# Kernel tuning notes

Hardware: AMD Instinct MI355X
Metric: run time of the kernel (lower is better)

Reference implementation:

```python
import jax, jax.numpy as jnp
import numpy as np

N, E, IN, HID, HEADS, OUT = 50000, 800000, 128, 32, 4, 2
NEG = 0.2   # LeakyReLU negative slope (PyG default)
EPS = 1e-5  # BatchNorm eps


def setup_inputs() -> dict:
    key = jax.random.key(0)
    ks = jax.random.split(key, 32)
    g = lambda i, shape, s=0.05: (jax.random.normal(ks[i], shape, jnp.float32) * s)
    d = {
        'x': jax.random.normal(ks[0], (N, IN), jnp.float32),
        'edge_index': jax.random.randint(ks[1], (2, E), 0, N, jnp.int32),
        'edge_attr': jax.random.normal(ks[2], (E, 1), jnp.float32),
        # conv1: GATv2, in=IN, out=HID, heads=HEADS, edge_dim=1
        'c1_Wl': g(3, (IN, HEADS * HID)), 'c1_bl': g(4, (HEADS * HID,)),
        'c1_Wr': g(5, (IN, HEADS * HID)), 'c1_br': g(6, (HEADS * HID,)),
        'c1_We': g(7, (1, HEADS * HID)),
        'c1_att': g(8, (HEADS, HID)),
        'c1_bias': g(9, (HEADS * HID,)),
        'bn1_gamma': jnp.ones((HEADS * HID,), jnp.float32),
        'bn1_beta': jnp.zeros((HEADS * HID,), jnp.float32),
        'bn1_mean': g(10, (HEADS * HID,)),
        'bn1_var': jax.random.uniform(ks[11], (HEADS * HID,), jnp.float32, 0.5, 1.5),
        # conv2: GATv2, in=HEADS*HID, out=HID, heads=1, edge_dim=1
        'c2_Wl': g(12, (HEADS * HID, HID)), 'c2_bl': g(13, (HID,)),
        'c2_Wr': g(14, (HEADS * HID, HID)), 'c2_br': g(15, (HID,)),
        'c2_We': g(16, (1, HID)),
        'c2_att': g(17, (1, HID)),
        'c2_bias': g(18, (HID,)),
        'bn2_gamma': jnp.ones((HID,), jnp.float32),
        'bn2_beta': jnp.zeros((HID,), jnp.float32),
        'bn2_mean': g(19, (HID,)),
        'bn2_var': jax.random.uniform(ks[20], (HID,), jnp.float32, 0.5, 1.5),
        # classifier
        'clf_W': g(21, (HID, OUT)), 'clf_b': g(22, (OUT,)),
    }
    return d


def _gatv2(x, src, dst, eattr, Wl, bl, Wr, br, We, att, bias, heads, out_ch, concat):
    n = x.shape[0]
    xl = (x @ Wl + bl).reshape(n, heads, out_ch)   # source transform
    xr = (x @ Wr + br).reshape(n, heads, out_ch)   # target transform
    el = (eattr @ We).reshape(-1, heads, out_ch)   # edge transform (no bias in PyG)
    s = xl[src] + xr[dst] + el                     # [E, H, C]
    s = jnp.where(s > 0, s, NEG * s)               # LeakyReLU
    logits = jnp.einsum('ehc,hc->eh', s, att)      # [E, H]
    # segment softmax over destination nodes (every node has a self-loop)
    m = jax.ops.segment_max(logits, dst, num_segments=n)
    a = jnp.exp(logits - m[dst])
    denom = jax.ops.segment_sum(a, dst, num_segments=n)
    alpha = a / denom[dst]                         # [E, H]
    out = jax.ops.segment_sum(alpha[:, :, None] * xl[src], dst, num_segments=n)
    out = out.reshape(n, heads * out_ch) if concat else out.mean(axis=1)
    return out + bias


def _bn_eval(x, gamma, beta, mean, var):
    return (x - mean) * (gamma / jnp.sqrt(var + EPS)) + beta


def reference(x, edge_index, edge_attr,
              c1_Wl, c1_bl, c1_Wr, c1_br, c1_We, c1_att, c1_bias,
              bn1_gamma, bn1_beta, bn1_mean, bn1_var,
              c2_Wl, c2_bl, c2_Wr, c2_br, c2_We, c2_att, c2_bias,
              bn2_gamma, bn2_beta, bn2_mean, bn2_var,
              clf_W, clf_b):
    n = x.shape[0]
    # add self-loops once (PyG GATv2 default add_self_loops=True, fill_value='mean')
    loop = jnp.arange(n, dtype=edge_index.dtype)
    src = jnp.concatenate([edge_index[0], loop])
    dst = jnp.concatenate([edge_index[1], loop])
    loop_attr = jnp.broadcast_to(edge_attr.mean(axis=0, keepdims=True), (n, edge_attr.shape[1]))
    eattr = jnp.concatenate([edge_attr, loop_attr], axis=0)

    h = _gatv2(x, src, dst, eattr, c1_Wl, c1_bl, c1_Wr, c1_br, c1_We, c1_att, c1_bias,
               HEADS, HID, True)
    h = jax.nn.relu(_bn_eval(h, bn1_gamma, bn1_beta, bn1_mean, bn1_var))
    # dropout inactive in eval mode
    h = _gatv2(h, src, dst, eattr, c2_Wl, c2_bl, c2_Wr, c2_br, c2_We, c2_att, c2_bias,
               1, HID, True)
    h = jax.nn.relu(_bn_eval(h, bn2_gamma, bn2_beta, bn2_mean, bn2_var))
    return h @ clf_W + clf_b
```

## Files before the change

kernel.cpp:

```cpp
#include <hip/hip_runtime.h>

#define NNODES 50000
#define NEDGES 800000
#define ETOT   850000
#define IN_CH  128
#define HID    32
#define HEADS  4
#define C1     128
#define NEG    0.2f
#define BNEPS  1e-5f
#define XFB2   1563
#define EHB    3125
#define WTS    160
#define XSS    136
#define NC     16
#define SCB    196

typedef __attribute__((ext_vector_type(8))) short short8;
typedef __attribute__((ext_vector_type(4))) float f32x4;

__device__ __forceinline__ unsigned short bf16r(float f) {
    unsigned u = __float_as_uint(f);
    return (unsigned short)((u + 0x7fffu + ((u >> 16) & 1u)) >> 16);
}
__device__ __forceinline__ unsigned bf16pair(float f0, float f1) {
    return (unsigned)bf16r(f0) | ((unsigned)bf16r(f1) << 16);
}
__device__ __forceinline__ float blo(unsigned u) { return __uint_as_float(u << 16); }
__device__ __forceinline__ float bhi(unsigned u) { return __uint_as_float(u & 0xffff0000u); }

__device__ __forceinline__ int block_iscan(int v, int* ls) {
    int lane = threadIdx.x & 63, w = threadIdx.x >> 6;
    #pragma unroll
    for (int o = 1; o < 64; o <<= 1) {
        int t = __shfl_up(v, o);
        if (lane >= o) v += t;
    }
    if (lane == 63) ls[w] = v;
    __syncthreads();
    int add = 0;
    #pragma unroll
    for (int i = 0; i < 4; i++) add += (i < w) ? ls[i] : 0;
    return v + add;
}

__global__ __launch_bounds__(256) void k_prep(const float* __restrict__ Wl1,
                                              const float* __restrict__ Wr1,
                                              const float* __restrict__ Wl2,
                                              const float* __restrict__ Wr2,
                                              unsigned short* __restrict__ WT,
                                              unsigned short* __restrict__ WT2) {
    int idx = blockIdx.x * 256 + threadIdx.x;
    if (idx < 32768) {
        int mat = idx >> 14, rem = idx & 16383;
        int k = rem >> 7, n = rem & 127;
        float v = mat ? Wr1[k * 128 + n] : Wl1[k * 128 + n];
        WT[(size_t)(mat * 128 + n) * WTS + k] = bf16r(v);
    } else {
        int i2 = idx - 32768;
        int mat = i2 >> 12, rem = i2 & 4095;
        int k = rem >> 5, n = rem & 31;
        float v = mat ? Wr2[k * 32 + n] : Wl2[k * 32 + n];
        WT2[(size_t)(mat * 32 + n) * WTS + k] = bf16r(v);
    }
}

__global__ __launch_bounds__(256) void k_xf_eh(
    const float* __restrict__ x,
    const float* __restrict__ bl, const float* __restrict__ br,
    const unsigned short* __restrict__ WT,
    unsigned* __restrict__ xlb, float* __restrict__ xr,
    const int* __restrict__ ei, const float* __restrict__ ea,
    int* __restrict__ hist, float* __restrict__ meanbuf) {
    __shared__ short xs_s[64 * XSS];
    if (blockIdx.x >= XFB2) {
        float* ls = (float*)xs_s;
        int eb = blockIdx.x - XFB2;
        int e = eb * 256 + threadIdx.x;
        int c = eb & (NC - 1);
        float v = 0.f;
        if (e < NEDGES) {
            atomicAdd(&hist[c * NNODES + ei[NEDGES + e]], 1);
            v = ea[e];
        }
        #pragma unroll
        for (int o = 32; o > 0; o >>= 1) v += __shfl_down(v, o, 64);
        if ((threadIdx.x & 63) == 0) ls[threadIdx.x >> 6] = v;
        __syncthreads();
        if (threadIdx.x == 0) atomicAdd(meanbuf, ls[0] + ls[1] + ls[2] + ls[3]);
        return;
    }
    int n0g = blockIdx.x * 32;
    {
        int nd = threadIdx.x >> 3, kc = (threadIdx.x & 7) * 16;
        bool valid = (n0g + nd) < NNODES;
        float xv[16];
        #pragma unroll
        for (int i = 0; i < 4; i++) {
            float4 t = valid ? ((const float4*)(x + (size_t)(n0g + nd) * IN_CH + kc))[i]
                             : make_float4(0.f, 0.f, 0.f, 0.f);
            xv[4 * i] = t.x; xv[4 * i + 1] = t.y; xv[4 * i + 2] = t.z; xv[4 * i + 3] = t.w;
        }
        unsigned hi[8], lo[8];
        #pragma unroll
        for (int i = 0; i < 8; i++) {
            unsigned short h0 = bf16r(xv[2 * i]), h1 = bf16r(xv[2 * i + 1]);
            float l0 = xv[2 * i]     - __uint_as_float(((unsigned)h0) << 16);
            float l1 = xv[2 * i + 1] - __uint_as_float(((unsigned)h1) << 16);
            hi[i] = (unsigned)h0 | ((unsigned)h1 << 16);
            lo[i] = bf16pair(l0, l1);
        }
        uint4* ph = (uint4*)&xs_s[nd * XSS + kc];
        ph[0] = make_uint4(hi[0], hi[1], hi[2], hi[3]);
        ph[1] = make_uint4(hi[4], hi[5], hi[6], hi[7]);
        uint4* pl = (uint4*)&xs_s[(nd + 32) * XSS + kc];
        pl[0] = make_uint4(lo[0], lo[1], lo[2], lo[3]);
        pl[1] = make_uint4(lo[4], lo[5], lo[6], lo[7]);
    }
    __syncthreads();
    int lane = threadIdx.x & 63;
    int lm = lane & 15, q = lane >> 4;
    int w = threadIdx.x >> 6;
    int n0 = w * 64;
    f32x4 acc[2][4];
    #pragma unroll
    for (int mt = 0; mt < 2; mt++)
        #pragma unroll
        for (int nt = 0; nt < 4; nt++) acc[mt][nt] = (f32x4)0.f;

    #pragma unroll
    for (int ks = 0; ks < 4; ks++) {
        int k0 = ks * 32 + q * 8;
        short8 ah0 = *(const short8*)&xs_s[(lm)      * XSS + k0];
        short8 ah1 = *(const short8*)&xs_s[(16 + lm) * XSS + k0];
        short8 al0 = *(const short8*)&xs_s[(32 + lm) * XSS + k0];
        short8 al1 = *(const short8*)&xs_s[(48 + lm) * XSS + k0];
        #pragma unroll
        for (int nt = 0; nt < 4; nt++) {
            short8 bfr = *(const short8*)(WT + (size_t)(n0 + nt * 16 + lm) * WTS + k0);
            acc[0][nt] = __builtin_amdgcn_mfma_f32_16x16x32_bf16(al0, bfr, acc[0][nt], 0, 0, 0);
            acc[0][nt] = __builtin_amdgcn_mfma_f32_16x16x32_bf16(ah0, bfr, acc[0][nt], 0, 0, 0);
            acc[1][nt] = __builtin_amdgcn_mfma_f32_16x16x32_bf16(al1, bfr, acc[1][nt], 0, 0, 0);
            acc[1][nt] = __builtin_amdgcn_mfma_f32_16x16x32_bf16(ah1, bfr, acc[1][nt], 0, 0, 0);
        }
    }
    if (w < 2) {
        #pragma unroll
        for (int nt = 0; nt < 4; nt++) {
            int ch = n0 + nt * 16 + lm;
            float bv = bl[ch];
            #pragma unroll
            for (int mt = 0; mt < 2; mt++)
                #pragma unroll
                for (int r = 0; r < 4; r++) {
                    int node = n0g + mt * 16 + q * 4 + r;
                    float val = acc[mt][nt][r] + bv;
                    float pv = __shfl_xor(val, 1);
                    if ((lm & 1) == 0 && node < NNODES)
                        xlb[(size_t)node * 64 + (ch >> 1)] = bf16pair(val, pv);
                }
        }
    } else {
        #pragma unroll
        for (int nt = 0; nt < 4; nt++) {
            int ch = n0 - 128 + nt * 16 + lm;
            float bv = br[ch];
            #pragma unroll
            for (int mt = 0; mt < 2; mt++)
                #pragma unroll
                for (int r = 0; r < 4; r++) {
                    int node = n0g + mt * 16 + q * 4 + r;
                    if (node < NNODES)
                        xr[(size_t)node * C1 + ch] = acc[mt][nt][r] + bv;
                }
        }
    }
}

__global__ __launch_bounds__(256) void k_red(int* __restrict__ hist,
                                             int* __restrict__ deg,
                                             int* __restrict__ bsum) {
    __shared__ int ls[4];
    int d = blockIdx.x * 256 + threadIdx.x;
    int s = 0;
    if (d < NNODES) {
        #pragma unroll
        for (int c = 0; c < NC; c++) {
            int v = hist[c * NNODES + d];
            hist[c * NNODES + d] = s;
            s += v;
        }
        deg[d] = s;
    }
    int v = (d < NNODES) ? s + 1 : 0;
    #pragma unroll
    for (int o = 32; o > 0; o >>= 1) v += __shfl_down(v, o, 64);
    if ((threadIdx.x & 63) == 0) ls[threadIdx.x >> 6] = v;
    __syncthreads();
    if (threadIdx.x == 0) bsum[blockIdx.x] = ls[0] + ls[1] + ls[2] + ls[3];
}

__global__ __launch_bounds__(256) void k_bscan(const int* __restrict__ bsum,
                                               int* __restrict__ boff) {
    __shared__ int ls[4];
    int t = threadIdx.x;
    int v = (t < SCB) ? bsum[t] : 0;
    int incl = block_iscan(v, ls);
    if (t < SCB) boff[t] = incl - v;
}

__global__ __launch_bounds__(256) void k_rowp(const int* __restrict__ deg,
                                              const int* __restrict__ boff,
                                              int* __restrict__ rowptr) {
    __shared__ int ls[4];
    int d = blockIdx.x * 256 + threadIdx.x;
    int v = (d < NNODES) ? deg[d] + 1 : 0;
    int incl = block_iscan(v, ls);
    int base = boff[blockIdx.x];
    if (d < NNODES) rowptr[d] = base + incl - v;
    if (d == NNODES - 1) rowptr[NNODES] = base + incl;
}

__global__ __launch_bounds__(256) void k_fill(const int* __restrict__ ei,
                                              const float* __restrict__ ea,
                                              const int* __restrict__ rowptr,
                                              const float* __restrict__ meanbuf,
                                              int* __restrict__ hist,
                                              unsigned* __restrict__ cpack) {
    int e = blockIdx.x * 256 + threadIdx.x;
    if (e < NEDGES) {
        int d = ei[NEDGES + e];
        int c = (e >> 8) & (NC - 1);
        int off = atomicAdd(&hist[c * NNODES + d], 1);
        cpack[rowptr[d] + 1 + off] = ((unsigned)bf16r(ea[e]) << 16) | (unsigned)ei[e];
    } else if (e < NEDGES + NNODES) {
        int i = e - NEDGES;
        cpack[rowptr[i]] = ((unsigned)bf16r(meanbuf[0] * (1.0f / NEDGES)) << 16) | (unsigned)i;
    } else if (e < NEDGES + NNODES + 64) {
        cpack[ETOT + e - NEDGES - NNODES] = 0u;
    }
}

__global__ __launch_bounds__(256) void k_edge1(
    const unsigned* __restrict__ xlb, const float* __restrict__ xr,
    const int* __restrict__ rowptr, const unsigned* __restrict__ cpack,
    const float* __restrict__ We, const float* __restrict__ att,
    float* __restrict__ out1) {
    int node = blockIdx.x * 4 + (threadIdx.x >> 6);
    if (node >= NNODES) return;
    int lane = threadIdx.x & 63;
    int q = lane & 15, s = lane >> 4;
    int r0 = rowptr[node], r1 = rowptr[node + 1];
    float4 xr0 = ((const float4*)xr)[(size_t)node * 32 + 2 * q];
    float4 xr1 = ((const float4*)xr)[(size_t)node * 32 + 2 * q + 1];
    float4 we0 = ((const float4*)We)[2 * q],  we1 = ((const float4*)We)[2 * q + 1];
    float4 at0 = ((const float4*)att)[2 * q], at1 = ((const float4*)att)[2 * q + 1];
    const uint4* xlv = (const uint4*)xlb;

    float den = 0.f;
    float a0 = 0.f, a1 = 0.f, a2 = 0.f, a3 = 0.f;
    float a4 = 0.f, a5 = 0.f, a6 = 0.f, a7 = 0.f;
    int nit = (r1 - r0 + 3) >> 2;
    int k = r0 + s;
    unsigned sc = cpack[k];
    uint4 xv = xlv[(size_t)(sc & 0xffffu) * 16 + q];
    for (int it = 0; it < nit; it++) {
        unsigned scn = cpack[k + 4];
        uint4 xvn = xlv[(size_t)(scn & 0xffffu) * 16 + q];
        bool ok = k < r1;
        float av = __uint_as_float(sc & 0xffff0000u);
        float x0 = blo(xv.x), x1 = bhi(xv.x), x2 = blo(xv.y), x3 = bhi(xv.y);
        float x4 = blo(xv.z), x5 = bhi(xv.z), x6 = blo(xv.w), x7 = bhi(xv.w);
        float v0 = x0 + xr0.x + av * we0.x;  v0 = v0 > 0.f ? v0 : NEG * v0;
        float v1 = x1 + xr0.y + av * we0.y;  v1 = v1 > 0.f ? v1 : NEG * v1;
        float v2 = x2 + xr0.z + av * we0.z;  v2 = v2 > 0.f ? v2 : NEG * v2;
        float v3 = x3 + xr0.w + av * we0.w;  v3 = v3 > 0.f ? v3 : NEG * v3;
        float v4 = x4 + xr1.x + av * we1.x;  v4 = v4 > 0.f ? v4 : NEG * v4;
        float v5 = x5 + xr1.y + av * we1.y;  v5 = v5 > 0.f ? v5 : NEG * v5;
        float v6 = x6 + xr1.z + av * we1.z;  v6 = v6 > 0.f ? v6 : NEG * v6;
        float v7 = x7 + xr1.w + av * we1.w;  v7 = v7 > 0.f ? v7 : NEG * v7;
        float t = v0 * at0.x + v1 * at0.y + v2 * at0.z + v3 * at0.w
                + v4 * at1.x + v5 * at1.y + v6 * at1.z + v7 * at1.w;
        t += __shfl_xor(t, 1);
        t += __shfl_xor(t, 2);
        float e = ok ? __expf(t) : 0.f;
        den += e;
        a0 = fmaf(e, x0, a0); a1 = fmaf(e, x1, a1);
        a2 = fmaf(e, x2, a2); a3 = fmaf(e, x3, a3);
        a4 = fmaf(e, x4, a4); a5 = fmaf(e, x5, a5);
        a6 = fmaf(e, x6, a6); a7 = fmaf(e, x7, a7);
        k += 4; sc = scn; xv = xvn;
    }
    #pragma unroll
    for (int o = 16; o <= 32; o <<= 1) {
        den += __shfl_xor(den, o);
        a0 += __shfl_xor(a0, o); a1 += __shfl_xor(a1, o);
        a2 += __shfl_xor(a2, o); a3 += __shfl_xor(a3, o);
        a4 += __shfl_xor(a4, o); a5 += __shfl_xor(a5, o);
        a6 += __shfl_xor(a6, o); a7 += __shfl_xor(a7, o);
    }
    if (s == 0) {
        float rd = 1.f / den;
        ((float4*)out1)[(size_t)node * 32 + 2 * q] =
            make_float4(a0 * rd, a1 * rd, a2 * rd, a3 * rd);
        ((float4*)out1)[(size_t)node * 32 + 2 * q + 1] =
            make_float4(a4 * rd, a5 * rd, a6 * rd, a7 * rd);
    }
}

__global__ __launch_bounds__(256) void k_epi(
    const float* __restrict__ out1, const float* __restrict__ bias1,
    const float* __restrict__ g1, const float* __restrict__ b1,
    const float* __restrict__ m1, const float* __restrict__ v1,
    const unsigned short* __restrict__ WT2,
    const float* __restrict__ bl2, const float* __restrict__ br2,
    unsigned* __restrict__ xlb2, float* __restrict__ xr2) {
    __shared__ short hs_s[64 * XSS];
    __shared__ float A[128], B[128];
    int n0g = blockIdx.x * 32;
    if (threadIdx.x < 128) {
        int c = threadIdx.x;
        float sc = g1[c] * rsqrtf(v1[c] + BNEPS);
        A[c] = sc;
        B[c] = (bias1[c] - m1[c]) * sc + b1[c];
    }
    __syncthreads();
    {
        int nd = threadIdx.x >> 3, kc = (threadIdx.x & 7) * 16;
        bool valid = (n0g + nd) < NNODES;
        float xv[16];
        #pragma unroll
        for (int i = 0; i < 4; i++) {
            float4 t = valid ? ((const float4*)(out1 + (size_t)(n0g + nd) * C1 + kc))[i]
                             : make_float4(0.f, 0.f, 0.f, 0.f);
            xv[4 * i] = t.x; xv[4 * i + 1] = t.y; xv[4 * i + 2] = t.z; xv[4 * i + 3] = t.w;
        }
        #pragma unroll
        for (int j = 0; j < 16; j++)
            xv[j] = fmaxf(xv[j] * A[kc + j] + B[kc + j], 0.f);
        unsigned hi[8], lo[8];
        #pragma unroll
        for (int i = 0; i < 8; i++) {
            unsigned short h0 = bf16r(xv[2 * i]), h1 = bf16r(xv[2 * i + 1]);
            float l0 = xv[2 * i]     - __uint_as_float(((unsigned)h0) << 16);
            float l1 = xv[2 * i + 1] - __uint_as_float(((unsigned)h1) << 16);
            hi[i] = (unsigned)h0 | ((unsigned)h1 << 16);
            lo[i] = bf16pair(l0, l1);
        }
        uint4* ph = (uint4*)&hs_s[nd * XSS + kc];
        ph[0] = make_uint4(hi[0], hi[1], hi[2], hi[3]);
        ph[1] = make_uint4(hi[4], hi[5], hi[6], hi[7]);
        uint4* pl = (uint4*)&hs_s[(nd + 32) * XSS + kc];
        pl[0] = make_uint4(lo[0], lo[1], lo[2], lo[3]);
        pl[1] = make_uint4(lo[4], lo[5], lo[6], lo[7]);
    }
    __syncthreads();
    int lane = threadIdx.x & 63;
    int lm = lane & 15, q = lane >> 4;
    int w = threadIdx.x >> 6;
    f32x4 acc[2];
    acc[0] = (f32x4)0.f; acc[1] = (f32x4)0.f;
    #pragma unroll
    for (int ks = 0; ks < 4; ks++) {
        int k0 = ks * 32 + q * 8;
        short8 ah0 = *(const short8*)&hs_s[(lm)      * XSS + k0];
        short8 ah1 = *(const short8*)&hs_s[(16 + lm) * XSS + k0];
        short8 al0 = *(const short8*)&hs_s[(32 + lm) * XSS + k0];
        short8 al1 = *(const short8*)&hs_s[(48 + lm) * XSS + k0];
        short8 bfr = *(const short8*)(WT2 + (size_t)(w * 16 + lm) * WTS + k0);
        acc[0] = __builtin_amdgcn_mfma_f32_16x16x32_bf16(al0, bfr, acc[0], 0, 0, 0);
        acc[0] = __builtin_amdgcn_mfma_f32_16x16x32_bf16(ah0, bfr, acc[0], 0, 0, 0);
        acc[1] = __builtin_amdgcn_mfma_f32_16x16x32_bf16(al1, bfr, acc[1], 0, 0, 0);
        acc[1] = __builtin_amdgcn_mfma_f32_16x16x32_bf16(ah1, bfr, acc[1], 0, 0, 0);
    }
    if (w < 2) {
        int ch = w * 16 + lm;
        float bv = bl2[ch];
        #pragma unroll
        for (int mt = 0; mt < 2; mt++)
            #pragma unroll
            for (int r = 0; r < 4; r++) {
                int node = n0g + mt * 16 + q * 4 + r;
                float val = acc[mt][r] + bv;
                float pv = __shfl_xor(val, 1);
                if ((lm & 1) == 0 && node < NNODES)
                    xlb2[(size_t)node * 16 + (ch >> 1)] = bf16pair(val, pv);
            }
    } else {
        int ch = (w - 2) * 16 + lm;
        float bv = br2[ch];
        #pragma unroll
        for (int mt = 0; mt < 2; mt++)
            #pragma unroll
            for (int r = 0; r < 4; r++) {
                int node = n0g + mt * 16 + q * 4 + r;
                if (node < NNODES)
                    xr2[(size_t)node * HID + ch] = acc[mt][r] + bv;
            }
    }
}

__global__ __launch_bounds__(256) void k_edge2(
    const unsigned* __restrict__ xlb2, const float* __restrict__ xr2,
    const int* __restrict__ rowptr, const unsigned* __restrict__ cpack,
    const float* __restrict__ We2, const float* __restrict__ att2,
    const float* __restrict__ bias2,
    const float* __restrict__ g2, const float* __restrict__ b2,
    const float* __restrict__ m2, const float* __restrict__ v2,
    const float* __restrict__ W, const float* __restrict__ b,
    float* __restrict__ y) {
    int node = blockIdx.x * 4 + (threadIdx.x >> 6);
    if (node >= NNODES) return;
    int lane = threadIdx.x & 63;
    int q = lane & 3, s = lane >> 2;
    int r0 = rowptr[node], r1 = rowptr[node + 1];
    float4 xr0 = ((const float4*)xr2)[(size_t)node * 8 + 2 * q];
    float4 xr1 = ((const float4*)xr2)[(size_t)node * 8 + 2 * q + 1];
    float4 we0 = ((const float4*)We2)[2 * q],  we1 = ((const float4*)We2)[2 * q + 1];
    float4 at0 = ((const float4*)att2)[2 * q], at1 = ((const float4*)att2)[2 * q + 1];
    const uint4* xlv = (const uint4*)xlb2;

    float den = 0.f;
    float a0 = 0.f, a1 = 0.f, a2 = 0.f, a3 = 0.f;
    float a4 = 0.f, a5 = 0.f, a6 = 0.f, a7 = 0.f;
    int nit = (r1 - r0 + 15) >> 4;
    int k = r0 + s;
    unsigned sc = cpack[k];
    uint4 xv = xlv[(size_t)(sc & 0xffffu) * 4 + q];
    for (int it = 0; it < nit; it++) {
        unsigned scn = cpack[k + 16];
        uint4 xvn = xlv[(size_t)(scn & 0xffffu) * 4 + q];
        bool ok = k < r1;
        float av = __uint_as_float(sc & 0xffff0000u);
        float x0 = blo(xv.x), x1 = bhi(xv.x), x2 = blo(xv.y), x3 = bhi(xv.y);
        float x4 = blo(xv.z), x5 = bhi(xv.z), x6 = blo(xv.w), x7 = bhi(xv.w);
        float v0 = x0 + xr0.x + av * we0.x;  v0 = v0 > 0.f ? v0 : NEG * v0;
        float v1 = x1 + xr0.y + av * we0.y;  v1 = v1 > 0.f ? v1 : NEG * v1;
        float v2 = x2 + xr0.z + av * we0.z;  v2 = v2 > 0.f ? v2 : NEG * v2;
        float v3 = x3 + xr0.w + av * we0.w;  v3 = v3 > 0.f ? v3 : NEG * v3;
        float v4 = x4 + xr1.x + av * we1.x;  v4 = v4 > 0.f ? v4 : NEG * v4;
        float v5 = x5 + xr1.y + av * we1.y;  v5 = v5 > 0.f ? v5 : NEG * v5;
        float v6 = x6 + xr1.z + av * we1.z;  v6 = v6 > 0.f ? v6 : NEG * v6;
        float v7 = x7 + xr1.w + av * we1.w;  v7 = v7 > 0.f ? v7 : NEG * v7;
        float t = v0 * at0.x + v1 * at0.y + v2 * at0.z + v3 * at0.w
                + v4 * at1.x + v5 * at1.y + v6 * at1.z + v7 * at1.w;
        t += __shfl_xor(t, 1);
        t += __shfl_xor(t, 2);
        float e = ok ? __expf(t) : 0.f;
        den += e;
        a0 = fmaf(e, x0, a0); a1 = fmaf(e, x1, a1);
        a2 = fmaf(e, x2, a2); a3 = fmaf(e, x3, a3);
        a4 = fmaf(e, x4, a4); a5 = fmaf(e, x5, a5);
        a6 = fmaf(e, x6, a6); a7 = fmaf(e, x7, a7);
        k += 16; sc = scn; xv = xvn;
    }
    #pragma unroll
    for (int o = 4; o <= 32; o <<= 1) {
        den += __shfl_xor(den, o);
        a0 += __shfl_xor(a0, o); a1 += __shfl_xor(a1, o);
        a2 += __shfl_xor(a2, o); a3 += __shfl_xor(a3, o);
        a4 += __shfl_xor(a4, o); a5 += __shfl_xor(a5, o);
        a6 += __shfl_xor(a6, o); a7 += __shfl_xor(a7, o);
    }
    float rd = 1.f / den;
    float4 gv0 = ((const float4*)g2)[2 * q],    gv1 = ((const float4*)g2)[2 * q + 1];
    float4 bv0 = ((const float4*)b2)[2 * q],    bv1 = ((const float4*)b2)[2 * q + 1];
    float4 mv0 = ((const float4*)m2)[2 * q],    mv1 = ((const float4*)m2)[2 * q + 1];
    float4 vv0 = ((const float4*)v2)[2 * q],    vv1 = ((const float4*)v2)[2 * q + 1];
    float4 bi0 = ((const float4*)bias2)[2 * q], bi1 = ((const float4*)bias2)[2 * q + 1];
    float h0 = (a0 * rd + bi0.x - mv0.x) * (gv0.x * rsqrtf(vv0.x + BNEPS)) + bv0.x;
    float h1 = (a1 * rd + bi0.y - mv0.y) * (gv0.y * rsqrtf(vv0.y + BNEPS)) + bv0.y;
    float h2 = (a2 * rd + bi0.z - mv0.z) * (gv0.z * rsqrtf(vv0.z + BNEPS)) + bv0.z;
    float h3 = (a3 * rd + bi0.w - mv0.w) * (gv0.w * rsqrtf(vv0.w + BNEPS)) + bv0.w;
    float h4 = (a4 * rd + bi1.x - mv1.x) * (gv1.x * rsqrtf(vv1.x + BNEPS)) + bv1.x;
    float h5 = (a5 * rd + bi1.y - mv1.y) * (gv1.y * rsqrtf(vv1.y + BNEPS)) + bv1.y;
    float h6 = (a6 * rd + bi1.z - mv1.z) * (gv1.z * rsqrtf(vv1.z + BNEPS)) + bv1.z;
    float h7 = (a7 * rd + bi1.w - mv1.w) * (gv1.w * rsqrtf(vv1.w + BNEPS)) + bv1.w;
    h0 = fmaxf(h0, 0.f); h1 = fmaxf(h1, 0.f); h2 = fmaxf(h2, 0.f); h3 = fmaxf(h3, 0.f);
    h4 = fmaxf(h4, 0.f); h5 = fmaxf(h5, 0.f); h6 = fmaxf(h6, 0.f); h7 = fmaxf(h7, 0.f);
    float4 w0 = ((const float4*)W)[4 * q];
    float4 w1 = ((const float4*)W)[4 * q + 1];
    float4 w2 = ((const float4*)W)[4 * q + 2];
    float4 w3 = ((const float4*)W)[4 * q + 3];
    float t0 = h0 * w0.x + h1 * w0.z + h2 * w1.x + h3 * w1.z
             + h4 * w2.x + h5 * w2.z + h6 * w3.x + h7 * w3.z;
    float t1 = h0 * w0.y + h1 * w0.w + h2 * w1.y + h3 * w1.w
             + h4 * w2.y + h5 * w2.w + h6 * w3.y + h7 * w3.w;
    t0 += __shfl_xor(t0, 1); t0 += __shfl_xor(t0, 2);
    t1 += __shfl_xor(t1, 1); t1 += __shfl_xor(t1, 2);
    if (lane == 0) {
        y[(size_t)node * 2]     = t0 + b[0];
        y[(size_t)node * 2 + 1] = t1 + b[1];
    }
}

extern "C" void kernel_launch(void* const* d_in, const int* in_sizes, int n_in,
                              void* d_out, int out_size, void* d_ws, size_t ws_size,
                              hipStream_t stream) {
    const float* x       = (const float*)d_in[0];
    const int*   ei      = (const int*)d_in[1];
    const float* ea      = (const float*)d_in[2];
    const float* c1_Wl   = (const float*)d_in[3];
    const float* c1_bl   = (const float*)d_in[4];
    const float* c1_Wr   = (const float*)d_in[5];
    const float* c1_br   = (const float*)d_in[6];
    const float* c1_We   = (const float*)d_in[7];
    const float* c1_att  = (const float*)d_in[8];
    const float* c1_bias = (const float*)d_in[9];
    const float* bn1_g   = (const float*)d_in[10];
    const float* bn1_b   = (const float*)d_in[11];
    const float* bn1_m   = (const float*)d_in[12];
    const float* bn1_v   = (const float*)d_in[13];
    const float* c2_Wl   = (const float*)d_in[14];
    const float* c2_bl   = (const float*)d_in[15];
    const float* c2_Wr   = (const float*)d_in[16];
    const float* c2_br   = (const float*)d_in[17];
    const float* c2_We   = (const float*)d_in[18];
    const float* c2_att  = (const float*)d_in[19];
    const float* c2_bias = (const float*)d_in[20];
    const float* bn2_g   = (const float*)d_in[21];
    const float* bn2_b   = (const float*)d_in[22];
    const float* bn2_m   = (const float*)d_in[23];
    const float* bn2_v   = (const float*)d_in[24];
    const float* clf_W   = (const float*)d_in[25];
    const float* clf_b   = (const float*)d_in[26];

    float* ws = (float*)d_ws;
    size_t off = 0;
    unsigned* XLb  = (unsigned*)(ws + off); off += (size_t)NNODES * 64;
    float*    XR1  = ws + off; off += (size_t)NNODES * C1;
    float*    OUT1 = ws + off; off += (size_t)NNODES * C1;
    unsigned* XLb2 = (unsigned*)(ws + off); off += (size_t)NNODES * 16;
    float*    XR2  = ws + off; off += (size_t)NNODES * HID;
    unsigned* CPACK= (unsigned*)(ws + off); off += (size_t)ETOT + 64;
    unsigned short* WT  = (unsigned short*)(ws + off); off += 256 * WTS / 2;
    unsigned short* WT2 = (unsigned short*)(ws + off); off += 64 * WTS / 2;
    int*      ROWP = (int*)(ws + off); off += NNODES + 16;
    int*      DEG  = (int*)(ws + off); off += NNODES;
    int*      BSUM = (int*)(ws + off); off += 256;
    int*      BOFF = (int*)(ws + off); off += 256;
    int*      HIST = (int*)(ws + off); off += (size_t)NC * NNODES;
    float*    MEANB= ws + off; off += 64;
    if (ws_size < off * sizeof(float)) return;

    hipMemsetAsync(HIST, 0, ((size_t)NC * NNODES + 64) * sizeof(int), stream);
    k_prep  <<<160, 256, 0, stream>>>(c1_Wl, c1_Wr, c2_Wl, c2_Wr, WT, WT2);
    k_xf_eh <<<XFB2 + EHB, 256, 0, stream>>>(x, c1_bl, c1_br, WT, XLb, XR1,
                                             ei, ea, HIST, MEANB);
    k_red   <<<SCB, 256, 0, stream>>>(HIST, DEG, BSUM);
    k_bscan <<<1, 256, 0, stream>>>(BSUM, BOFF);
    k_rowp  <<<SCB, 256, 0, stream>>>(DEG, BOFF, ROWP);
    k_fill  <<<(NEDGES + NNODES + 64 + 255) / 256, 256, 0, stream>>>(ei, ea, ROWP, MEANB, HIST, CPACK);
    k_edge1 <<<(NNODES + 3) / 4, 256, 0, stream>>>(XLb, XR1, ROWP, CPACK, c1_We, c1_att, OUT1);
    k_epi   <<<XFB2, 256, 0, stream>>>(OUT1, c1_bias, bn1_g, bn1_b, bn1_m, bn1_v,
                                       WT2, c2_bl, c2_br, XLb2, XR2);
    k_edge2 <<<(NNODES + 3) / 4, 256, 0, stream>>>(XLb2, XR2, ROWP, CPACK, c2_We, c2_att,
                                                   c2_bias, bn2_g, bn2_b, bn2_m, bn2_v,
                                                   clf_W, clf_b, (float*)d_out);
}
```

Baseline: 338.6 us.

## Replace global atomic CSR build with two-level bucket sort by destination block

The CSR construction no longer uses global-memory atomic histograms over 16 copies of the node array. It now does a per-block shared-memory histogram over 196 coarse destination buckets, scans those counts, scatters edges into buckets, and then sorts each bucket locally in shared memory to produce rowptr and the packed edge list. The large memset is removed, and its zeroing work moves into k_prep. In exchange the build adds an 8-byte-per-edge intermediate bucket buffer and one more pass over the edges, and the bucket order within each node is no longer deterministic.

```diff
diff --git a/kernel.cpp b/kernel.cpp
--- a/kernel.cpp
+++ b/kernel.cpp
@@ -5,7 +5,6 @@
 #define ETOT   850000
 #define IN_CH  128
 #define HID    32
-#define HEADS  4
 #define C1     128
 #define NEG    0.2f
 #define BNEPS  1e-5f
@@ -13,8 +12,8 @@
 #define EHB    3125
 #define WTS    160
 #define XSS    136
-#define NC     16
-#define SCB    196
+#define NB     196
+#define THS    3136
 
 typedef __attribute__((ext_vector_type(8))) short short8;
 typedef __attribute__((ext_vector_type(4))) float f32x4;
@@ -49,8 +48,14 @@
                                               const float* __restrict__ Wl2,
                                               const float* __restrict__ Wr2,
                                               unsigned short* __restrict__ WT,
-                                              unsigned short* __restrict__ WT2) {
+                                              unsigned short* __restrict__ WT2,
+                                              float* __restrict__ meanbuf,
+                                              unsigned* __restrict__ cpack) {
     int idx = blockIdx.x * 256 + threadIdx.x;
+    if (blockIdx.x == 0) {
+        if (threadIdx.x == 0) meanbuf[0] = 0.f;
+        if (threadIdx.x < 64) cpack[ETOT + threadIdx.x] = 0u;
+    }
     if (idx < 32768) {
         int mat = idx >> 14, rem = idx & 16383;
         int k = rem >> 7, n = rem & 127;
@@ -71,23 +76,27 @@
     const unsigned short* __restrict__ WT,
     unsigned* __restrict__ xlb, float* __restrict__ xr,
     const int* __restrict__ ei, const float* __restrict__ ea,
-    int* __restrict__ hist, float* __restrict__ meanbuf) {
+    int* __restrict__ TH, float* __restrict__ meanbuf) {
     __shared__ short xs_s[64 * XSS];
     if (blockIdx.x >= XFB2) {
-        float* ls = (float*)xs_s;
-        int eb = blockIdx.x - XFB2;
-        int e = eb * 256 + threadIdx.x;
-        int c = eb & (NC - 1);
+        int* ih = (int*)xs_s;
+        float* ls = (float*)(ih + 200);
+        int hb = blockIdx.x - XFB2;
+        int t = threadIdx.x;
+        if (t < NB) ih[t] = 0;
+        __syncthreads();
+        int e = hb * 256 + t;
         float v = 0.f;
         if (e < NEDGES) {
-            atomicAdd(&hist[c * NNODES + ei[NEDGES + e]], 1);
+            atomicAdd(&ih[ei[NEDGES + e] >> 8], 1);
             v = ea[e];
         }
         #pragma unroll
         for (int o = 32; o > 0; o >>= 1) v += __shfl_down(v, o, 64);
-        if ((threadIdx.x & 63) == 0) ls[threadIdx.x >> 6] = v;
+        if ((t & 63) == 0) ls[t >> 6] = v;
         __syncthreads();
-        if (threadIdx.x == 0) atomicAdd(meanbuf, ls[0] + ls[1] + ls[2] + ls[3]);
+        if (t < NB) TH[(size_t)t * THS + hb] = ih[t];
+        if (t == 0) atomicAdd(meanbuf, ls[0] + ls[1] + ls[2] + ls[3]);
         return;
     }
     int n0g = blockIdx.x * 32;
@@ -177,67 +186,90 @@
     }
 }
 
-__global__ __launch_bounds__(256) void k_red(int* __restrict__ hist,
-                                             int* __restrict__ deg,
-                                             int* __restrict__ bsum) {
+__global__ __launch_bounds__(256) void k_scan1(int* __restrict__ TH,
+                                               int* __restrict__ btot) {
     __shared__ int ls[4];
-    int d = blockIdx.x * 256 + threadIdx.x;
-    int s = 0;
-    if (d < NNODES) {
-        #pragma unroll
-        for (int c = 0; c < NC; c++) {
-            int v = hist[c * NNODES + d];
-            hist[c * NNODES + d] = s;
-            s += v;
-        }
-        deg[d] = s;
-    }
-    int v = (d < NNODES) ? s + 1 : 0;
-    #pragma unroll
-    for (int o = 32; o > 0; o >>= 1) v += __shfl_down(v, o, 64);
-    if ((threadIdx.x & 63) == 0) ls[threadIdx.x >> 6] = v;
-    __syncthreads();
-    if (threadIdx.x == 0) bsum[blockIdx.x] = ls[0] + ls[1] + ls[2] + ls[3];
-}
-
-__global__ __launch_bounds__(256) void k_bscan(const int* __restrict__ bsum,
-                                               int* __restrict__ boff) {
+    __shared__ int carry;
+    int b = blockIdx.x, t = threadIdx.x;
+    size_t base = (size_t)b * THS;
+    if (t == 0) carry = 0;
+    __syncthreads();
+    for (int c0 = 0; c0 < 3328; c0 += 256) {
+        int idx = c0 + t;
+        int v = (idx < EHB) ? TH[base + idx] : 0;
+        int incl = block_iscan(v, ls);
+        int run = carry;
+        __syncthreads();
+        if (idx < EHB) TH[base + idx] = run + incl - v;
+        if (t == 255) carry = run + incl;
+        __syncthreads();
+    }
+    if (t == 0) btot[b] = carry;
+}
+
+__global__ __launch_bounds__(256) void k_scan2(const int* __restrict__ btot,
+                                               int* __restrict__ bbe) {
     __shared__ int ls[4];
     int t = threadIdx.x;
-    int v = (t < SCB) ? bsum[t] : 0;
+    int v = (t < NB) ? btot[t] : 0;
     int incl = block_iscan(v, ls);
-    if (t < SCB) boff[t] = incl - v;
-}
-
-__global__ __launch_bounds__(256) void k_rowp(const int* __restrict__ deg,
-                                              const int* __restrict__ boff,
-                                              int* __restrict__ rowptr) {
-    __shared__ int ls[4];
-    int d = blockIdx.x * 256 + threadIdx.x;
-    int v = (d < NNODES) ? deg[d] + 1 : 0;
+    if (t < NB) bbe[t] = incl - v;
+}
+
+__global__ __launch_bounds__(256) void k_fill2(const int* __restrict__ ei,
+                                               const float* __restrict__ ea,
+                                               const int* __restrict__ TH,
+                                               const int* __restrict__ bbe,
+                                               uint2* __restrict__ buck) {
+    __shared__ int thl[NB];
+    __shared__ int rk[NB];
+    int blk = blockIdx.x, t = threadIdx.x;
+    if (t < NB) {
+        thl[t] = bbe[t] + TH[(size_t)t * THS + blk];
+        rk[t] = 0;
+    }
+    __syncthreads();
+    int e = blk * 256 + t;
+    int dst = ei[NEDGES + e], src = ei[e];
+    int b = dst >> 8;
+    int r = atomicAdd(&rk[b], 1);
+    buck[thl[b] + r] = make_uint2(((unsigned)bf16r(ea[e]) << 16) | (unsigned)src,
+                                  (unsigned)(dst & 255));
+}
+
+__global__ __launch_bounds__(256) void k_bsort(const uint2* __restrict__ buck,
+                                               const int* __restrict__ bbe,
+                                               const int* __restrict__ btot,
+                                               const float* __restrict__ meanbuf,
+                                               int* __restrict__ rowptr,
+                                               unsigned* __restrict__ cpack) {
+    __shared__ int hist[256], Pl[256], ls[4];
+    int b = blockIdx.x, t = threadIdx.x;
+    int n0 = b * 256;
+    int ebase = bbe[b], ecnt = btot[b];
+    hist[t] = 0;
+    __syncthreads();
+    for (int i = t; i < ecnt; i += 256) atomicAdd(&hist[buck[ebase + i].y], 1);
+    __syncthreads();
+    bool valid = (n0 + t) < NNODES;
+    int deg = hist[t];
+    int v = valid ? deg + 1 : 0;
     int incl = block_iscan(v, ls);
-    int base = boff[blockIdx.x];
-    if (d < NNODES) rowptr[d] = base + incl - v;
-    if (d == NNODES - 1) rowptr[NNODES] = base + incl;
-}
-
-__global__ __launch_bounds__(256) void k_fill(const int* __restrict__ ei,
-                                              const float* __restrict__ ea,
-                                              const int* __restrict__ rowptr,
-                                              const float* __restrict__ meanbuf,
-                                              int* __restrict__ hist,
-                                              unsigned* __restrict__ cpack) {
-    int e = blockIdx.x * 256 + threadIdx.x;
-    if (e < NEDGES) {
-        int d = ei[NEDGES + e];
-        int c = (e >> 8) & (NC - 1);
-        int off = atomicAdd(&hist[c * NNODES + d], 1);
-        cpack[rowptr[d] + 1 + off] = ((unsigned)bf16r(ea[e]) << 16) | (unsigned)ei[e];
-    } else if (e < NEDGES + NNODES) {
-        int i = e - NEDGES;
-        cpack[rowptr[i]] = ((unsigned)bf16r(meanbuf[0] * (1.0f / NEDGES)) << 16) | (unsigned)i;
-    } else if (e < NEDGES + NNODES + 64) {
-        cpack[ETOT + e - NEDGES - NNODES] = 0u;
+    int P = incl - v;
+    Pl[t] = P;
+    int cb = ebase + n0;
+    if (valid) rowptr[n0 + t] = cb + P;
+    if (b == NB - 1 && t == 0) rowptr[NNODES] = ETOT;
+    if (valid)
+        cpack[cb + P] = ((unsigned)bf16r(meanbuf[0] * (1.0f / NEDGES)) << 16)
+                        | (unsigned)(n0 + t);
+    __syncthreads();
+    hist[t] = 0;
+    __syncthreads();
+    for (int i = t; i < ecnt; i += 256) {
+        uint2 ev = buck[ebase + i];
+        int r = atomicAdd(&hist[ev.y], 1);
+        cpack[cb + Pl[ev.y] + 1 + r] = ev.x;
     }
 }
 
@@ -535,22 +567,21 @@
     unsigned* CPACK= (unsigned*)(ws + off); off += (size_t)ETOT + 64;
     unsigned short* WT  = (unsigned short*)(ws + off); off += 256 * WTS / 2;
     unsigned short* WT2 = (unsigned short*)(ws + off); off += 64 * WTS / 2;
+    int*      TH   = (int*)(ws + off); off += (size_t)NB * THS;
+    int*      BTOT = (int*)(ws + off); off += 256;
+    int*      BBE  = (int*)(ws + off); off += 256;
+    uint2*    BUCK = (uint2*)(ws + off); off += (size_t)NEDGES * 2;
     int*      ROWP = (int*)(ws + off); off += NNODES + 16;
-    int*      DEG  = (int*)(ws + off); off += NNODES;
-    int*      BSUM = (int*)(ws + off); off += 256;
-    int*      BOFF = (int*)(ws + off); off += 256;
-    int*      HIST = (int*)(ws + off); off += (size_t)NC * NNODES;
     float*    MEANB= ws + off; off += 64;
     if (ws_size < off * sizeof(float)) return;
 
-    hipMemsetAsync(HIST, 0, ((size_t)NC * NNODES + 64) * sizeof(int), stream);
-    k_prep  <<<160, 256, 0, stream>>>(c1_Wl, c1_Wr, c2_Wl, c2_Wr, WT, WT2);
+    k_prep  <<<160, 256, 0, stream>>>(c1_Wl, c1_Wr, c2_Wl, c2_Wr, WT, WT2, MEANB, CPACK);
     k_xf_eh <<<XFB2 + EHB, 256, 0, stream>>>(x, c1_bl, c1_br, WT, XLb, XR1,
-                                             ei, ea, HIST, MEANB);
-    k_red   <<<SCB, 256, 0, stream>>>(HIST, DEG, BSUM);
-    k_bscan <<<1, 256, 0, stream>>>(BSUM, BOFF);
-    k_rowp  <<<SCB, 256, 0, stream>>>(DEG, BOFF, ROWP);
-    k_fill  <<<(NEDGES + NNODES + 64 + 255) / 256, 256, 0, stream>>>(ei, ea, ROWP, MEANB, HIST, CPACK);
+                                             ei, ea, TH, MEANB);
+    k_scan1 <<<NB, 256, 0, stream>>>(TH, BTOT);
+    k_scan2 <<<1, 256, 0, stream>>>(BTOT, BBE);
+    k_fill2 <<<EHB, 256, 0, stream>>>(ei, ea, TH, BBE, BUCK);
+    k_bsort <<<NB, 256, 0, stream>>>(BUCK, BBE, BTOT, MEANB, ROWP, CPACK);
     k_edge1 <<<(NNODES + 3) / 4, 256, 0, stream>>>(XLb, XR1, ROWP, CPACK, c1_We, c1_att, OUT1);
     k_epi   <<<XFB2, 256, 0, stream>>>(OUT1, c1_bias, bn1_g, bn1_b, bn1_m, bn1_v,
                                        WT2, c2_bl, c2_br, XLb2, XR2);
```

Result: faster. 308.3 us (-9.0%).
